# Kernel optimization log

Hardware: AMD Instinct MI355X
Metric: run time of the kernel (lower is better)

The kernel has to match this reference:

```python
import jax, jax.numpy as jnp
import numpy as np

B, A, C, M = 4, 120000, 80, 32
ALPHA, GAMMA, EPS = 0.75, 2.0, 1e-4
STD = np.array([0.1, 0.1, 0.2, 0.2, 0.1, 0.1, 0.2, 0.2], dtype=np.float32)


def _make_boxes(key, shape, img=1024.0):
    k1, k2, k3, k4 = jax.random.split(key, 4)
    cx = jax.random.uniform(k1, shape) * img
    cy = jax.random.uniform(k2, shape) * img
    w = jax.random.uniform(k3, shape) * 224.0 + 32.0
    h = jax.random.uniform(k4, shape) * 224.0 + 32.0
    return jnp.stack([cx - 0.5 * w, cy - 0.5 * h, cx + 0.5 * w, cy + 0.5 * h], axis=-1)


def setup_inputs() -> dict:
    key = jax.random.key(0)
    kc, kr, ka, kh, kf, kl, ki = jax.random.split(key, 7)
    classifications = jax.random.uniform(kc, (B, A, C), dtype=jnp.float32)
    regressions = jax.random.normal(kr, (B, A, 8), dtype=jnp.float32)
    anchors = _make_boxes(ka, (1, A))  # [1,A,4]
    head = _make_boxes(kh, (B, M))     # [B,M,4]
    full = _make_boxes(kf, (B, M))     # [B,M,4]
    labels = jax.random.randint(kl, (B, M, 1), 0, C).astype(jnp.float32)
    ignore = jax.random.randint(ki, (B, M, 1), 0, 2).astype(jnp.float32)
    annotations = jnp.concatenate([head, full, labels, ignore], axis=-1)  # [B,M,10]
    return {"classifications": classifications, "regressions": regressions,
            "anchors": anchors, "annotations": annotations}


def _calc_iou(a, b):
    # a: [A,4], b: [B,M,4] -> [B,A,M]
    area_b = (b[..., 2] - b[..., 0]) * (b[..., 3] - b[..., 1])  # [B,M]
    a = a[None, :, None, :]
    bb = b[:, None, :, :]
    iw = jnp.clip(jnp.minimum(a[..., 2], bb[..., 2]) - jnp.maximum(a[..., 0], bb[..., 0]), 0.0)
    ih = jnp.clip(jnp.minimum(a[..., 3], bb[..., 3]) - jnp.maximum(a[..., 1], bb[..., 1]), 0.0)
    area_a = ((a[..., 2] - a[..., 0]) * (a[..., 3] - a[..., 1]))  # [1,A,1]
    inter = iw * ih
    ua = jnp.clip(area_a + area_b[:, None, :] - inter, 1e-8)
    return inter / ua


def reference(classifications, regressions, anchors, annotations):
    anchor = anchors[0]                       # [A,4]
    aw = anchor[:, 2] - anchor[:, 0]
    ah = anchor[:, 3] - anchor[:, 1]
    acx = anchor[:, 0] + 0.5 * aw
    acy = anchor[:, 1] + 0.5 * ah

    ann = annotations[..., :-1]               # [B,M,9]
    full_box = ann[..., 4:8]

    iou = _calc_iou(anchor, full_box)         # [B,A,M]
    iou_max = jnp.max(iou, axis=-1)           # [B,A]
    iou_arg = jnp.argmax(iou, axis=-1)        # [B,A]

    pos = iou_max >= 0.5                      # [B,A]
    neg = iou_max < 0.4
    num_pos = jnp.sum(pos, axis=1).astype(jnp.float32)  # [B]

    assigned = jnp.take_along_axis(ann, iou_arg[..., None], axis=1)  # [B,A,9]
    assigned_cls = assigned[..., 8].astype(jnp.int32)                # [B,A]

    one_hot = jax.nn.one_hot(assigned_cls, classifications.shape[-1], dtype=jnp.float32)
    targets = jnp.where(pos[..., None], one_hot,
                        jnp.where(neg[..., None], 0.0, -1.0))        # [B,A,C]

    p = jnp.clip(classifications, EPS, 1.0 - EPS)
    alpha_f = jnp.where(targets == 1.0, ALPHA, 1.0 - ALPHA)
    focal_w = alpha_f * jnp.where(targets == 1.0, 1.0 - p, p) ** GAMMA
    bce = -(targets * jnp.log(p) + (1.0 - targets) * jnp.log(1.0 - p))
    cls_loss = jnp.where(targets != -1.0, focal_w * bce, 0.0)
    cls_losses = jnp.sum(cls_loss, axis=(1, 2)) / jnp.clip(num_pos, 1.0)  # [B]

    gw_h = assigned[..., 2] - assigned[..., 0]
    gh_h = assigned[..., 3] - assigned[..., 1]
    gcx_h = assigned[..., 0] + 0.5 * gw_h
    gcy_h = assigned[..., 1] + 0.5 * gh_h
    gw_f = assigned[..., 6] - assigned[..., 4]
    gh_f = assigned[..., 7] - assigned[..., 5]
    gcx_f = assigned[..., 4] + 0.5 * gw_f
    gcy_f = assigned[..., 5] + 0.5 * gh_f
    gw_h = jnp.clip(gw_h, 1.0); gh_h = jnp.clip(gh_h, 1.0)
    gw_f = jnp.clip(gw_f, 1.0); gh_f = jnp.clip(gh_f, 1.0)

    t = jnp.stack([
        (gcx_f - acx) / aw, (gcy_f - acy) / ah,
        jnp.log(gw_f / aw), jnp.log(gh_f / ah),
        (gcx_h - acx) / aw * 4.0, (gcy_h - acy) / ah * 4.0,
        jnp.log(gw_h / aw * 4.0), jnp.log(gh_h / ah * 4.0),
    ], axis=-1) / jnp.asarray(STD)            # [B,A,8]

    diff = jnp.abs(t - regressions)
    # only_full=True: weights zero out cols 4:8
    diff = diff * jnp.asarray([1., 1., 1., 1., 0., 0., 0., 0.], dtype=jnp.float32)
    rl = jnp.where(diff <= 1.0 / 9.0, 0.5 * 9.0 * diff * diff, diff - 0.5 / 9.0)
    rl4 = rl[..., 0:4] * pos[..., None]       # [B,A,4], only positive anchors
    reg_losses = jnp.where(num_pos > 0,
                           jnp.sum(rl4, axis=(1, 2)) / (jnp.clip(num_pos, 1.0) * 4.0),
                           0.0)               # mean over positive rows x 4 cols

    return (jnp.mean(cls_losses, keepdims=True), jnp.mean(reg_losses, keepdims=True))
```

## Files before the change

### kernel.cpp

```cpp
#include <hip/hip_runtime.h>

#define NB 4
#define NA 120000
#define NC 80
#define NM 32

#define EPS_   1e-4f
#define LN2_   0.69314718055994531f

constexpr int BLOCK  = 256;
constexpr int WPB    = 4;
constexpr int APW    = 16;
constexpr int APC    = WPB * APW;
constexpr int NCHUNK = NA / APC;
constexpr int BPB    = 512;
constexpr int BINS   = 64;

__device__ __forceinline__ float wave_reduce_f(float v) {
    #pragma unroll
    for (int off = 32; off > 0; off >>= 1) v += __shfl_down(v, off, 64);
    return v;
}
__device__ __forceinline__ double wave_reduce_d(double v) {
    #pragma unroll
    for (int off = 32; off > 0; off >>= 1) v += __shfl_down(v, off, 64);
    return v;
}

__device__ __forceinline__ float flog2(float x) { return __builtin_amdgcn_logf(x); }

__global__ __launch_bounds__(BLOCK, 4)
void focal_persist(const float* __restrict__ cls,
                   const float* __restrict__ reg,
                   const float* __restrict__ anchors,
                   const float* __restrict__ ann,
                   double* __restrict__ acc)
{
    __shared__ float s_ann[NM * 10];
    __shared__ float s_red[3][WPB];

    const int b    = blockIdx.x >> 9;
    const int blk  = blockIdx.x & (BPB - 1);
    const int tid  = threadIdx.x;
    const int wave = tid >> 6;
    const int lane = tid & 63;
    const int aloc = lane >> 2;
    const int part = lane & 3;

    s_ann[tid] = ann[b * NM * 10 + tid];
    if (tid < NM * 10 - BLOCK) s_ann[BLOCK + tid] = ann[b * NM * 10 + BLOCK + tid];
    __syncthreads();

    float clsSum = 0.0f, regLoss = 0.0f, posCnt = 0.0f;

    const float4* anchors4 = (const float4*)anchors;
    const float4* cls4b    = (const float4*)cls + (size_t)b * NA * (NC / 4);

    for (int c = blk; c < NCHUNK; c += BPB) {
        const int aw0 = c * APC + wave * APW;
        const int a   = aw0 + aloc;

        const float4 an = anchors4[a];
        const float4* w4 = cls4b + (size_t)aw0 * (NC / 4);
        float4 x0 = w4[lane];
        float4 x1 = w4[lane + 64];
        float4 x2 = w4[lane + 128];
        float4 x3 = w4[lane + 192];
        float4 x4_ = w4[lane + 256];

        const float ax1 = an.x, ay1 = an.y, ax2 = an.z, ay2 = an.w;
        const float aw_ = ax2 - ax1, ah = ay2 - ay1;
        const float acx = ax1 + 0.5f * aw_, acy = ay1 + 0.5f * ah;
        const float areaA = aw_ * ah;

        float best = -1.0f;
        int   arg  = 0;
        #pragma unroll
        for (int i = 0; i < 8; ++i) {
            const int m = part * 8 + i;
            const float bx1 = s_ann[m * 10 + 4];
            const float by1 = s_ann[m * 10 + 5];
            const float bx2 = s_ann[m * 10 + 6];
            const float by2 = s_ann[m * 10 + 7];
            float iw = fminf(ax2, bx2) - fmaxf(ax1, bx1); iw = fmaxf(iw, 0.0f);
            float ih = fminf(ay2, by2) - fmaxf(ay1, by1); ih = fmaxf(ih, 0.0f);
            const float inter = iw * ih;
            const float areaB = (bx2 - bx1) * (by2 - by1);
            const float ua    = fmaxf(areaA + areaB - inter, 1e-8f);
            const float iou   = inter / ua;
            if (iou > best) { best = iou; arg = m; }
        }
        #pragma unroll
        for (int d = 1; d <= 2; d <<= 1) {
            const float ob = __shfl_xor(best, d, 64);
            const int   oa = __shfl_xor(arg,  d, 64);
            if (ob > best || (ob == best && oa < arg)) { best = ob; arg = oa; }
        }

        const bool pos = best >= 0.5f;
        const bool neg = best < 0.4f;
        const float coefL = (pos || neg) ? (-0.25f * LN2_) : 0.0f;

        if (pos && part == 0) {
            posCnt += 1.0f;
            const int cc = (int)s_ann[arg * 10 + 8];
            const float xc = cls[((size_t)b * NA + a) * NC + cc];
            const float p  = fminf(fmaxf(xc, EPS_), 1.0f - EPS_);
            const float q  = 1.0f - p;
            clsSum += 0.75f * q * q * (-LN2_ * flog2(p))
                    - 0.25f * p * p * (-LN2_ * flog2(q));

            const float fx1 = s_ann[arg * 10 + 4];
            const float fy1 = s_ann[arg * 10 + 5];
            const float fx2 = s_ann[arg * 10 + 6];
            const float fy2 = s_ann[arg * 10 + 7];
            float gw = fx2 - fx1, gh = fy2 - fy1;
            const float gcx = fx1 + 0.5f * gw, gcy = fy1 + 0.5f * gh;
            gw = fmaxf(gw, 1.0f); gh = fmaxf(gh, 1.0f);
            const float t0 = ((gcx - acx) / aw_) * 10.0f;
            const float t1 = ((gcy - acy) / ah)  * 10.0f;
            const float t2 = (LN2_ * flog2(gw / aw_)) * 5.0f;
            const float t3 = (LN2_ * flog2(gh / ah))  * 5.0f;
            const float4 r4 = ((const float4*)reg)[(size_t)(b * NA + a) * 2];
            const float d0 = fabsf(t0 - r4.x);
            const float d1 = fabsf(t1 - r4.y);
            const float d2 = fabsf(t2 - r4.z);
            const float d3 = fabsf(t3 - r4.w);
            const float beta = 1.0f / 9.0f;
            #define SL1(d) ((d) <= beta ? 4.5f * (d) * (d) : (d) - 0.5f / 9.0f)
            regLoss += SL1(d0) + SL1(d1) + SL1(d2) + SL1(d3);
            #undef SL1
        }

        #define TERM(XV, J)                                                      \
        {                                                                        \
            const int idx = lane + 64 * (J);                                     \
            const float C = __shfl(coefL, (idx / (NC / 4)) << 2, 64);            \
            float p0 = fminf(fmaxf((XV).x, EPS_), 1.0f - EPS_);                  \
            float p1 = fminf(fmaxf((XV).y, EPS_), 1.0f - EPS_);                  \
            float p2 = fminf(fmaxf((XV).z, EPS_), 1.0f - EPS_);                  \
            float p3 = fminf(fmaxf((XV).w, EPS_), 1.0f - EPS_);                  \
            float t0 = p0 * p0 * flog2(1.0f - p0);                               \
            float t1 = p1 * p1 * flog2(1.0f - p1);                               \
            float t2 = p2 * p2 * flog2(1.0f - p2);                               \
            float t3 = p3 * p3 * flog2(1.0f - p3);                               \
            clsSum = fmaf((t0 + t1) + (t2 + t3), C, clsSum);                     \
        }
        TERM(x0, 0) TERM(x1, 1) TERM(x2, 2) TERM(x3, 3) TERM(x4_, 4)
        #undef TERM
    }

    float rc = wave_reduce_f(clsSum);
    float rr = wave_reduce_f(regLoss);
    float rp = wave_reduce_f(posCnt);
    if (lane == 0) { s_red[0][wave] = rc; s_red[1][wave] = rr; s_red[2][wave] = rp; }
    __syncthreads();
    if (tid == 0) {
        const float c = (s_red[0][0] + s_red[0][1]) + (s_red[0][2] + s_red[0][3]);
        const float r = (s_red[1][0] + s_red[1][1]) + (s_red[1][2] + s_red[1][3]);
        const float p = (s_red[2][0] + s_red[2][1]) + (s_red[2][2] + s_red[2][3]);
        const int bin = blockIdx.x & (BINS - 1);
        atomicAdd(&acc[(b * 3 + 0) * BINS + bin], (double)c);
        atomicAdd(&acc[(b * 3 + 1) * BINS + bin], (double)r);
        atomicAdd(&acc[(b * 3 + 2) * BINS + bin], (double)p);
    }
}

__global__ void focal_finalize(const double* __restrict__ acc, float* __restrict__ out) {
    __shared__ double g[NB * 3];
    const int tid  = threadIdx.x;
    const int wave = tid >> 6, lane = tid & 63;
    double v = acc[wave * BINS + lane];
    v = wave_reduce_d(v);
    if (lane == 0) g[wave] = v;
    __syncthreads();
    if (tid == 0) {
        double clsTot = 0.0, regTot = 0.0;
        #pragma unroll
        for (int b = 0; b < NB; ++b) {
            const double np  = g[b * 3 + 2];
            const double npc = np < 1.0 ? 1.0 : np;
            clsTot += g[b * 3 + 0] / npc;
            regTot += (np > 0.0) ? g[b * 3 + 1] / (npc * 4.0) : 0.0;
        }
        out[0] = (float)(clsTot / NB);
        out[1] = (float)(regTot / NB);
    }
}

extern "C" void kernel_launch(void* const* d_in, const int* in_sizes, int n_in,
                              void* d_out, int out_size, void* d_ws, size_t ws_size,
                              hipStream_t stream) {
    const float* cls     = (const float*)d_in[0];
    const float* reg     = (const float*)d_in[1];
    const float* anchors = (const float*)d_in[2];
    const float* ann     = (const float*)d_in[3];
    float* out  = (float*)d_out;
    double* acc = (double*)d_ws;

    hipMemsetAsync(acc, 0, NB * 3 * BINS * sizeof(double), stream);

    focal_persist<<<NB * BPB, BLOCK, 0, stream>>>(cls, reg, anchors, ann, acc);
    focal_finalize<<<1, NB * 3 * BINS, 0, stream>>>(acc, out);
}
```

Measured before the change: 232.7 us.

## Prefetch next chunk into registers and defer positive-anchor work to a shared queue

The main loop now loads the next chunk's anchor and classification float4s before computing the current chunk, so global-load latency overlaps with the IoU and focal-loss math. The divergent per-positive branch (gather of the target class score, regression targets, smooth-L1) is removed from the loop. Instead, positive anchors are pushed into a shared-memory queue via a shared atomic and processed by one thread each after the loop. The positive count comes from the queue length. This adds register pressure from the double-buffered loads and relies on the queue (capacity 256) never overflowing, which holds because each block covers at most 256 anchors per batch.

```diff
diff --git a/kernel.cpp b/kernel.cpp
--- a/kernel.cpp
+++ b/kernel.cpp
@@ -15,6 +15,7 @@
 constexpr int NCHUNK = NA / APC;
 constexpr int BPB    = 512;
 constexpr int BINS   = 64;
+constexpr int QCAP   = 256;
 
 __device__ __forceinline__ float wave_reduce_f(float v) {
     #pragma unroll
@@ -37,7 +38,9 @@
                    double* __restrict__ acc)
 {
     __shared__ float s_ann[NM * 10];
-    __shared__ float s_red[3][WPB];
+    __shared__ float s_red[2][WPB];
+    __shared__ int   s_q[QCAP];
+    __shared__ int   s_qn;
 
     const int b    = blockIdx.x >> 9;
     const int blk  = blockIdx.x & (BPB - 1);
@@ -47,31 +50,38 @@
     const int aloc = lane >> 2;
     const int part = lane & 3;
 
+    if (tid == 0) s_qn = 0;
     s_ann[tid] = ann[b * NM * 10 + tid];
     if (tid < NM * 10 - BLOCK) s_ann[BLOCK + tid] = ann[b * NM * 10 + BLOCK + tid];
     __syncthreads();
 
-    float clsSum = 0.0f, regLoss = 0.0f, posCnt = 0.0f;
+    float clsSum = 0.0f, regLoss = 0.0f;
 
     const float4* anchors4 = (const float4*)anchors;
     const float4* cls4b    = (const float4*)cls + (size_t)b * NA * (NC / 4);
 
-    for (int c = blk; c < NCHUNK; c += BPB) {
+    int c = blk;
+    float4 an0, x0, x1, x2, x3, x4_;
+    {
         const int aw0 = c * APC + wave * APW;
-        const int a   = aw0 + aloc;
-
-        const float4 an = anchors4[a];
+        an0 = anchors4[aw0 + aloc];
         const float4* w4 = cls4b + (size_t)aw0 * (NC / 4);
-        float4 x0 = w4[lane];
-        float4 x1 = w4[lane + 64];
-        float4 x2 = w4[lane + 128];
-        float4 x3 = w4[lane + 192];
-        float4 x4_ = w4[lane + 256];
-
-        const float ax1 = an.x, ay1 = an.y, ax2 = an.z, ay2 = an.w;
-        const float aw_ = ax2 - ax1, ah = ay2 - ay1;
-        const float acx = ax1 + 0.5f * aw_, acy = ay1 + 0.5f * ah;
-        const float areaA = aw_ * ah;
+        x0 = w4[lane]; x1 = w4[lane + 64]; x2 = w4[lane + 128];
+        x3 = w4[lane + 192]; x4_ = w4[lane + 256];
+    }
+
+    while (c < NCHUNK) {
+        const int cn = c + BPB;
+        const int cl  = (cn < NCHUNK) ? cn : c;
+        const int nw0 = cl * APC + wave * APW;
+        const float4 an1 = anchors4[nw0 + aloc];
+        const float4* v4 = cls4b + (size_t)nw0 * (NC / 4);
+        const float4 y0 = v4[lane], y1 = v4[lane + 64], y2 = v4[lane + 128];
+        const float4 y3 = v4[lane + 192], y4 = v4[lane + 256];
+
+        const int a = c * APC + wave * APW + aloc;
+        const float ax1 = an0.x, ay1 = an0.y, ax2 = an0.z, ay2 = an0.w;
+        const float areaA = (ax2 - ax1) * (ay2 - ay1);
 
         float best = -1.0f;
         int   arg  = 0;
@@ -102,34 +112,8 @@
         const float coefL = (pos || neg) ? (-0.25f * LN2_) : 0.0f;
 
         if (pos && part == 0) {
-            posCnt += 1.0f;
-            const int cc = (int)s_ann[arg * 10 + 8];
-            const float xc = cls[((size_t)b * NA + a) * NC + cc];
-            const float p  = fminf(fmaxf(xc, EPS_), 1.0f - EPS_);
-            const float q  = 1.0f - p;
-            clsSum += 0.75f * q * q * (-LN2_ * flog2(p))
-                    - 0.25f * p * p * (-LN2_ * flog2(q));
-
-            const float fx1 = s_ann[arg * 10 + 4];
-            const float fy1 = s_ann[arg * 10 + 5];
-            const float fx2 = s_ann[arg * 10 + 6];
-            const float fy2 = s_ann[arg * 10 + 7];
-            float gw = fx2 - fx1, gh = fy2 - fy1;
-            const float gcx = fx1 + 0.5f * gw, gcy = fy1 + 0.5f * gh;
-            gw = fmaxf(gw, 1.0f); gh = fmaxf(gh, 1.0f);
-            const float t0 = ((gcx - acx) / aw_) * 10.0f;
-            const float t1 = ((gcy - acy) / ah)  * 10.0f;
-            const float t2 = (LN2_ * flog2(gw / aw_)) * 5.0f;
-            const float t3 = (LN2_ * flog2(gh / ah))  * 5.0f;
-            const float4 r4 = ((const float4*)reg)[(size_t)(b * NA + a) * 2];
-            const float d0 = fabsf(t0 - r4.x);
-            const float d1 = fabsf(t1 - r4.y);
-            const float d2 = fabsf(t2 - r4.z);
-            const float d3 = fabsf(t3 - r4.w);
-            const float beta = 1.0f / 9.0f;
-            #define SL1(d) ((d) <= beta ? 4.5f * (d) * (d) : (d) - 0.5f / 9.0f)
-            regLoss += SL1(d0) + SL1(d1) + SL1(d2) + SL1(d3);
-            #undef SL1
+            const int slot = atomicAdd(&s_qn, 1);
+            s_q[slot] = (a << 5) | arg;
         }
 
         #define TERM(XV, J)                                                      \
@@ -148,21 +132,62 @@
         }
         TERM(x0, 0) TERM(x1, 1) TERM(x2, 2) TERM(x3, 3) TERM(x4_, 4)
         #undef TERM
+
+        c = cn;
+        an0 = an1; x0 = y0; x1 = y1; x2 = y2; x3 = y3; x4_ = y4;
+    }
+
+    __syncthreads();
+    const int qn = s_qn;
+    if (tid < qn) {
+        const int e = s_q[tid];
+        const int a = e >> 5;
+        const int m = e & 31;
+
+        const float4 an = anchors4[a];
+        const float aw_ = an.z - an.x, ah = an.w - an.y;
+        const float acx = an.x + 0.5f * aw_, acy = an.y + 0.5f * ah;
+
+        const int cc = (int)s_ann[m * 10 + 8];
+        const float xc = cls[((size_t)b * NA + a) * NC + cc];
+        const float p  = fminf(fmaxf(xc, EPS_), 1.0f - EPS_);
+        const float q  = 1.0f - p;
+        clsSum += 0.75f * q * q * (-LN2_ * flog2(p))
+                - 0.25f * p * p * (-LN2_ * flog2(q));
+
+        const float fx1 = s_ann[m * 10 + 4];
+        const float fy1 = s_ann[m * 10 + 5];
+        const float fx2 = s_ann[m * 10 + 6];
+        const float fy2 = s_ann[m * 10 + 7];
+        float gw = fx2 - fx1, gh = fy2 - fy1;
+        const float gcx = fx1 + 0.5f * gw, gcy = fy1 + 0.5f * gh;
+        gw = fmaxf(gw, 1.0f); gh = fmaxf(gh, 1.0f);
+        const float t0 = ((gcx - acx) / aw_) * 10.0f;
+        const float t1 = ((gcy - acy) / ah)  * 10.0f;
+        const float t2 = (LN2_ * flog2(gw / aw_)) * 5.0f;
+        const float t3 = (LN2_ * flog2(gh / ah))  * 5.0f;
+        const float4 r4 = ((const float4*)reg)[(size_t)(b * NA + a) * 2];
+        const float d0 = fabsf(t0 - r4.x);
+        const float d1 = fabsf(t1 - r4.y);
+        const float d2 = fabsf(t2 - r4.z);
+        const float d3 = fabsf(t3 - r4.w);
+        const float beta = 1.0f / 9.0f;
+        #define SL1(d) ((d) <= beta ? 4.5f * (d) * (d) : (d) - 0.5f / 9.0f)
+        regLoss = SL1(d0) + SL1(d1) + SL1(d2) + SL1(d3);
+        #undef SL1
     }
 
     float rc = wave_reduce_f(clsSum);
     float rr = wave_reduce_f(regLoss);
-    float rp = wave_reduce_f(posCnt);
-    if (lane == 0) { s_red[0][wave] = rc; s_red[1][wave] = rr; s_red[2][wave] = rp; }
+    if (lane == 0) { s_red[0][wave] = rc; s_red[1][wave] = rr; }
     __syncthreads();
     if (tid == 0) {
-        const float c = (s_red[0][0] + s_red[0][1]) + (s_red[0][2] + s_red[0][3]);
-        const float r = (s_red[1][0] + s_red[1][1]) + (s_red[1][2] + s_red[1][3]);
-        const float p = (s_red[2][0] + s_red[2][1]) + (s_red[2][2] + s_red[2][3]);
+        const float cs = (s_red[0][0] + s_red[0][1]) + (s_red[0][2] + s_red[0][3]);
+        const float rs = (s_red[1][0] + s_red[1][1]) + (s_red[1][2] + s_red[1][3]);
         const int bin = blockIdx.x & (BINS - 1);
-        atomicAdd(&acc[(b * 3 + 0) * BINS + bin], (double)c);
-        atomicAdd(&acc[(b * 3 + 1) * BINS + bin], (double)r);
-        atomicAdd(&acc[(b * 3 + 2) * BINS + bin], (double)p);
+        atomicAdd(&acc[(b * 3 + 0) * BINS + bin], (double)cs);
+        atomicAdd(&acc[(b * 3 + 1) * BINS + bin], (double)rs);
+        atomicAdd(&acc[(b * 3 + 2) * BINS + bin], (double)qn);
     }
 }
 
```

Measured after the change: 232.6 us. Within noise of the previous version (-0.0%).
